# Performance work log

Hardware: AMD Instinct MI355X
Metric: run time of the kernel (lower is better)

Reference implementation:

```python
import jax, jax.numpy as jnp
import numpy as np
import math

B, S, HID, H = 2, 1024, 768, 12
D = HID // H  # 64
ALPHA = 32.0


def setup_inputs() -> dict:
    key = jax.random.key(0)
    ks = jax.random.split(key, 8)
    return {
        "hidden_states": jax.random.normal(ks[0], (B, S, HID), jnp.float32),
        "attention_mask": jnp.zeros((B, 1, 1, S), jnp.float32),
        "head_mask": jnp.ones((1, H, 1, 1), jnp.float32),
        "rel_pos": jax.random.normal(ks[1], (B, H, S, S), jnp.float32),
        "rel_2d_pos": jax.random.normal(ks[2], (B, H, S, S), jnp.float32),
        "Wq": jax.random.normal(ks[3], (HID, HID), jnp.float32) * 0.02,
        "bq": jnp.zeros((HID,), jnp.float32),
        "Wk": jax.random.normal(ks[4], (HID, HID), jnp.float32) * 0.02,
        "bk": jnp.zeros((HID,), jnp.float32),
        "Wv": jax.random.normal(ks[5], (HID, HID), jnp.float32) * 0.02,
        "bv": jnp.zeros((HID,), jnp.float32),
    }


def _heads(x):
    # [B,S,HID] -> [B,H,S,D]
    return x.reshape(B, S, H, D).transpose(0, 2, 1, 3)


def cogview_softmax(scores, alpha=ALPHA):
    s = scores / alpha
    m = jnp.max(s, axis=-1, keepdims=True)
    return jax.nn.softmax((s - m) * alpha, axis=-1)


def reference(hidden_states, attention_mask, head_mask, rel_pos, rel_2d_pos,
              Wq, bq, Wk, bk, Wv, bv):
    norm = math.sqrt(D)
    q = _heads(hidden_states @ Wq + bq) / norm   # [B,H,S,D]
    k = _heads(hidden_states @ Wk + bk)
    v = _heads(hidden_states @ Wv + bv)
    scores = jnp.einsum("bhsd,bhtd->bhst", q, k)
    scores = scores + (rel_pos + rel_2d_pos) / norm
    scores = scores + attention_mask
    probs = cogview_softmax(scores)              # [B,H,S,S]
    probs = probs * head_mask
    ctx = jnp.einsum("bhst,bhtd->bhsd", probs, v)
    ctx = ctx.transpose(0, 2, 1, 3).reshape(B, S, HID)
    return ctx
```

## Files before the change

kernel.cpp:

```cpp
#include <hip/hip_runtime.h>
#include <hip/hip_bf16.h>
#include <cstdint>

#define BB   2
#define SS   1024
#define HIDD 768
#define NH   12
#define DH   64
#define BH   (BB*NH)

typedef short bf16x8 __attribute__((ext_vector_type(8)));
typedef float f32x4  __attribute__((ext_vector_type(4)));

__device__ __forceinline__ unsigned short f2b(float x) {
    union { float f; uint32_t u; } v; v.f = x;
    uint32_t u = v.u;
    uint32_t r = (u + 0x7fffu + ((u >> 16) & 1u)) >> 16;
    return (unsigned short)r;
}

__device__ __forceinline__ void async16(const void* g, void* l) {
    __builtin_amdgcn_global_load_lds(
        (const __attribute__((address_space(1))) unsigned int*)g,
        (__attribute__((address_space(3))) unsigned int*)l,
        16, 0, 0);
}

__global__ void cvt_x(const float* __restrict__ x, unsigned short* __restrict__ xb) {
    int i = blockIdx.x * blockDim.x + threadIdx.x;
    float4 v = ((const float4*)x)[i];
    ushort4 o;
    o.x = f2b(v.x); o.y = f2b(v.y); o.z = f2b(v.z); o.w = f2b(v.w);
    ((ushort4*)xb)[i] = o;
}

__global__ void transpose_w(const float* __restrict__ Wq, const float* __restrict__ Wk,
                            const float* __restrict__ Wv, unsigned short* __restrict__ Wt) {
    __shared__ float tile[32][33];
    const int w = blockIdx.z;
    const float* W = (w == 0) ? Wq : (w == 1) ? Wk : Wv;
    const int tx = threadIdx.x & 31, ty = threadIdx.x >> 5;
    const int k0 = blockIdx.x * 32, n0 = blockIdx.y * 32;
    for (int p = 0; p < 4; ++p)
        tile[ty + p * 8][tx] = W[(k0 + ty + p * 8) * HIDD + n0 + tx];
    __syncthreads();
    for (int p = 0; p < 4; ++p) {
        int n = n0 + ty + p * 8;
        Wt[(w * HIDD + n) * HIDD + k0 + tx] = f2b(tile[tx][ty + p * 8]);
    }
}

__global__ __launch_bounds__(256) void qkv_gemm(
    const unsigned short* __restrict__ Xb, const unsigned short* __restrict__ Wt,
    const float* __restrict__ bq, const float* __restrict__ bk, const float* __restrict__ bv,
    unsigned short* __restrict__ Qh, unsigned short* __restrict__ Kh,
    unsigned short* __restrict__ Vh) {
    __shared__ __align__(16) unsigned short lA[2][128 * 32];
    __shared__ __align__(16) unsigned short lB[2][64 * 32];
    const int t = threadIdx.x;
    const int wave = t >> 6, lane = t & 63;
    const int l15 = lane & 15, quad = lane >> 4;
    const int m0 = blockIdx.x * 128;
    const int n0 = blockIdx.y * 64;
    const int wm = wave * 32;

    f32x4 acc[2][4] = {};

    auto stage = [&](int k0, int b) {
        #pragma unroll
        for (int r = 0; r < 2; ++r) {
            int ci = r * 256 + t;
            async16(Xb + (m0 + (ci >> 2)) * HIDD + k0 + (ci & 3) * 8,
                    &lA[b][(r * 256 + wave * 64) * 8]);
        }
        async16(Wt + (n0 + (t >> 2)) * HIDD + k0 + (t & 3) * 8,
                &lB[b][(wave * 64) * 8]);
    };

    stage(0, 0);
    for (int ki = 0; ki < 24; ++ki) {
        const int cur = ki & 1;
        __syncthreads();
        if (ki < 23) stage((ki + 1) * 32, cur ^ 1);
        bf16x8 af[2], bf[4];
        #pragma unroll
        for (int i = 0; i < 2; ++i)
            af[i] = *(const bf16x8*)&lA[cur][(wm + i * 16 + l15) * 32 + quad * 8];
        #pragma unroll
        for (int j = 0; j < 4; ++j)
            bf[j] = *(const bf16x8*)&lB[cur][(j * 16 + l15) * 32 + quad * 8];
        #pragma unroll
        for (int i = 0; i < 2; ++i)
            #pragma unroll
            for (int j = 0; j < 4; ++j)
                acc[i][j] = __builtin_amdgcn_mfma_f32_16x16x32_bf16(af[i], bf[j], acc[i][j], 0, 0, 0);
    }

    const int sect = (n0 >= 1536) ? 2 : (n0 >= 768) ? 1 : 0;
    const float* bias = (sect == 0) ? bq : (sect == 1) ? bk : bv;
    unsigned short* dst = (sect == 0) ? Qh : (sect == 1) ? Kh : Vh;
    const float scale = (sect == 0) ? 0.125f : 1.0f;
    #pragma unroll
    for (int i = 0; i < 2; ++i) {
        #pragma unroll
        for (int j = 0; j < 4; ++j) {
            int n  = n0 + j * 16 + l15;
            int nn = n - sect * HIDD;
            int h = nn >> 6, d = nn & 63;
            float bval = bias[nn];
            #pragma unroll
            for (int r = 0; r < 4; ++r) {
                int m = m0 + wm + i * 16 + quad * 4 + r;
                int b = m >> 10, s = m & 1023;
                float v = (acc[i][j][r] + bval) * scale;
                dst[((size_t)(b * NH + h) * SS + s) * DH + d] = f2b(v);
            }
        }
    }
}

__global__ __launch_bounds__(256) void transpose_v(
    const unsigned short* __restrict__ Vh, unsigned short* __restrict__ VhT) {
    __shared__ unsigned short tile[64][65];
    const int t = threadIdx.x;
    const int bh = blockIdx.y;
    const int s0 = blockIdx.x * 64;
    const int tx = t & 63, ty = t >> 6;
    const unsigned short* src = Vh + (size_t)bh * SS * DH;
    #pragma unroll
    for (int p = 0; p < 16; ++p)
        tile[ty + p * 4][tx] = src[(size_t)(s0 + ty + p * 4) * DH + tx];
    __syncthreads();
    unsigned short* dst = VhT + (size_t)bh * DH * SS;
    #pragma unroll
    for (int p = 0; p < 16; ++p)
        dst[(size_t)(ty + p * 4) * SS + s0 + tx] = tile[tx][ty + p * 4];
}

__global__ __launch_bounds__(128) void flash_attn(
    const unsigned short* __restrict__ Qh, const unsigned short* __restrict__ Kh,
    const unsigned short* __restrict__ VhT,
    const float* __restrict__ rel, const float* __restrict__ rel2d,
    const float* __restrict__ amask, const float* __restrict__ hmask,
    float* __restrict__ out) {
    __shared__ __align__(16) char smemraw[53760];

    const int t = threadIdx.x;
    const int wave = t >> 6, lane = t & 63;
    const int l15 = lane & 15, quad = lane >> 4;
    const int l7 = l15 & 7;
    const int bh = blockIdx.y;
    const int b = bh / NH, h = bh % NH;
    const int m0w = blockIdx.x * 32 + wave * 16;

    const unsigned short* Qp = Qh + (size_t)bh * SS * DH;
    const unsigned short* Kp = Kh + (size_t)bh * SS * DH;
    const unsigned short* Vp = VhT + (size_t)bh * DH * SS;
    const float* relp  = rel   + (size_t)bh * SS * SS;
    const float* rel2p = rel2d + (size_t)bh * SS * SS;
    const float* maskp = amask + (size_t)b * SS;

    float* stgA = (float*)(smemraw + 32768 + wave * 8192);
    float* stgB = stgA + 1024;
    unsigned short* Pw = (unsigned short*)(smemraw + 49152) + wave * (16 * 72);

    auto stage_kv = [&](int j0, int buf) {
        unsigned short* dK = (unsigned short*)(smemraw + buf * 8192);
        unsigned short* dV = (unsigned short*)(smemraw + 16384 + buf * 8192);
        #pragma unroll
        for (int i = 0; i < 4; ++i) {
            int ci = i * 128 + t;
            int row = ci >> 3, sc = ci & 7;
            int g = sc ^ (row & 7);
            async16(Kp + (size_t)(j0 + row) * DH + g * 8,
                    dK + (i * 128 + wave * 64) * 8);
            async16(Vp + (size_t)row * SS + j0 + g * 8,
                    dV + (i * 128 + wave * 64) * 8);
        }
    };

    auto stage_bias = [&](int j0) {
        #pragma unroll
        for (int i = 0; i < 4; ++i) {
            async16(relp  + (size_t)(m0w + 4 * i + quad) * SS + j0 + l15 * 4,
                    (char*)stgA + i * 1024);
            async16(rel2p + (size_t)(m0w + 4 * i + quad) * SS + j0 + l15 * 4,
                    (char*)stgB + i * 1024);
        }
    };

    bf16x8 qf0 = *(const bf16x8*)&Qp[(m0w + l15) * DH + quad * 8];
    bf16x8 qf1 = *(const bf16x8*)&Qp[(m0w + l15) * DH + 32 + quad * 8];

    f32x4 o[4] = {};
    float mrow[4] = {-1e30f, -1e30f, -1e30f, -1e30f};
    float lrow[4] = {0.f, 0.f, 0.f, 0.f};

    stage_kv(0, 0);
    __syncthreads();

    for (int tt = 0; tt < 16; ++tt) {
        const int j0 = tt * 64, cur = tt & 1;
        const unsigned short* cK = (const unsigned short*)(smemraw + cur * 8192);
        const unsigned short* cV = (const unsigned short*)(smemraw + 16384 + cur * 8192);

        stage_bias(j0);
        if (tt < 15) stage_kv(j0 + 64, cur ^ 1);

        float mk[4];
        #pragma unroll
        for (int c = 0; c < 4; ++c) mk[c] = maskp[j0 + c * 16 + l15];

        f32x4 sc4[4] = {};
        #pragma unroll
        for (int c = 0; c < 4; ++c) {
            int row = c * 16 + l15;
            bf16x8 k0f = *(const bf16x8*)&cK[row * 64 + (quad ^ l7) * 8];
            bf16x8 k1f = *(const bf16x8*)&cK[row * 64 + ((quad + 4) ^ l7) * 8];
            sc4[c] = __builtin_amdgcn_mfma_f32_16x16x32_bf16(qf0, k0f, sc4[c], 0, 0, 0);
            sc4[c] = __builtin_amdgcn_mfma_f32_16x16x32_bf16(qf1, k1f, sc4[c], 0, 0, 0);
        }

        if (tt < 15) { asm volatile("s_waitcnt vmcnt(8)" ::: "memory"); }
        else         { asm volatile("s_waitcnt vmcnt(0)" ::: "memory"); }

        float sv[4][4];
        #pragma unroll
        for (int c = 0; c < 4; ++c)
            #pragma unroll
            for (int r = 0; r < 4; ++r) {
                int fi = (quad * 4 + r) * 64 + c * 16 + l15;
                sv[c][r] = sc4[c][r] + (stgA[fi] + stgB[fi]) * 0.125f + mk[c];
            }

        float alpha[4];
        #pragma unroll
        for (int r = 0; r < 4; ++r) {
            float mx = fmaxf(fmaxf(sv[0][r], sv[1][r]), fmaxf(sv[2][r], sv[3][r]));
            #pragma unroll
            for (int off = 1; off < 16; off <<= 1) mx = fmaxf(mx, __shfl_xor(mx, off, 64));
            float mnew = fmaxf(mrow[r], mx);
            alpha[r] = __expf(mrow[r] - mnew);
            mrow[r] = mnew;
            float rs = 0.f;
            #pragma unroll
            for (int c = 0; c < 4; ++c) {
                float p = __expf(sv[c][r] - mnew);
                sv[c][r] = p;
                rs += p;
            }
            #pragma unroll
            for (int off = 1; off < 16; off <<= 1) rs += __shfl_xor(rs, off, 64);
            lrow[r] = lrow[r] * alpha[r] + rs;
            o[0][r] *= alpha[r]; o[1][r] *= alpha[r]; o[2][r] *= alpha[r]; o[3][r] *= alpha[r];
        }

        #pragma unroll
        for (int c = 0; c < 4; ++c)
            #pragma unroll
            for (int r = 0; r < 4; ++r)
                Pw[(quad * 4 + r) * 72 + c * 16 + l15] = f2b(sv[c][r]);

        bf16x8 pf0 = *(const bf16x8*)&Pw[l15 * 72 + quad * 8];
        bf16x8 pf1 = *(const bf16x8*)&Pw[l15 * 72 + 32 + quad * 8];

        #pragma unroll
        for (int dt = 0; dt < 4; ++dt) {
            int row = dt * 16 + l15;
            bf16x8 v0f = *(const bf16x8*)&cV[row * 64 + (quad ^ l7) * 8];
            bf16x8 v1f = *(const bf16x8*)&cV[row * 64 + ((quad + 4) ^ l7) * 8];
            o[dt] = __builtin_amdgcn_mfma_f32_16x16x32_bf16(pf0, v0f, o[dt], 0, 0, 0);
            o[dt] = __builtin_amdgcn_mfma_f32_16x16x32_bf16(pf1, v1f, o[dt], 0, 0, 0);
        }

        __syncthreads();
    }

    const float hm = hmask[h];
    #pragma unroll
    for (int r = 0; r < 4; ++r) {
        float inv = hm / lrow[r];
        int s = m0w + quad * 4 + r;
        float* op = out + ((size_t)(b * SS + s)) * HIDD + h * DH;
        #pragma unroll
        for (int dt = 0; dt < 4; ++dt) op[dt * 16 + l15] = o[dt][r] * inv;
    }
}

extern "C" void kernel_launch(void* const* d_in, const int* in_sizes, int n_in,
                              void* d_out, int out_size, void* d_ws, size_t ws_size,
                              hipStream_t stream) {
    const float* hs    = (const float*)d_in[0];
    const float* am    = (const float*)d_in[1];
    const float* hm    = (const float*)d_in[2];
    const float* rel   = (const float*)d_in[3];
    const float* rel2d = (const float*)d_in[4];
    const float* Wq    = (const float*)d_in[5];
    const float* bq    = (const float*)d_in[6];
    const float* Wk    = (const float*)d_in[7];
    const float* bk    = (const float*)d_in[8];
    const float* Wv    = (const float*)d_in[9];
    const float* bv    = (const float*)d_in[10];
    float* out = (float*)d_out;

    unsigned short* Xb  = (unsigned short*)d_ws;
    unsigned short* Wt  = Xb + 2048 * HIDD;
    unsigned short* Qh  = Wt + 3 * HIDD * HIDD;
    unsigned short* Kh  = Qh + (size_t)BH * SS * DH;
    unsigned short* Vh  = Kh + (size_t)BH * SS * DH;
    unsigned short* VhT = Vh + (size_t)BH * SS * DH;

    cvt_x<<<(2048 * HIDD / 4) / 256, 256, 0, stream>>>(hs, Xb);
    dim3 gT(24, 24, 3);
    transpose_w<<<gT, 256, 0, stream>>>(Wq, Wk, Wv, Wt);
    dim3 gG(16, 36);
    qkv_gemm<<<gG, 256, 0, stream>>>(Xb, Wt, bq, bk, bv, Qh, Kh, Vh);
    dim3 gV(16, BH);
    transpose_v<<<gV, 256, 0, stream>>>(Vh, VhT);
    dim3 gF(32, BH);
    flash_attn<<<gF, 128, 0, stream>>>(Qh, Kh, VhT, rel, rel2d, am, hm, out);
}
```

Measured before the change: 274.7 us.

## Prefetch relative-position bias directly into registers instead of LDS staging

```diff
diff --git a/kernel.cpp b/kernel.cpp
--- a/kernel.cpp
+++ b/kernel.cpp
@@ -143,7 +143,7 @@
     const float* __restrict__ rel, const float* __restrict__ rel2d,
     const float* __restrict__ amask, const float* __restrict__ hmask,
     float* __restrict__ out) {
-    __shared__ __align__(16) char smemraw[53760];
+    __shared__ __align__(16) char smemraw[37376];
 
     const int t = threadIdx.x;
     const int wave = t >> 6, lane = t & 63;
@@ -160,9 +160,15 @@
     const float* rel2p = rel2d + (size_t)bh * SS * SS;
     const float* maskp = amask + (size_t)b * SS;
 
-    float* stgA = (float*)(smemraw + 32768 + wave * 8192);
-    float* stgB = stgA + 1024;
-    unsigned short* Pw = (unsigned short*)(smemraw + 49152) + wave * (16 * 72);
+    unsigned short* Pw = (unsigned short*)(smemraw + 32768) + wave * (16 * 72);
+
+    const float* rowA[4];
+    const float* rowB[4];
+    #pragma unroll
+    for (int r = 0; r < 4; ++r) {
+        rowA[r] = relp  + (size_t)(m0w + quad * 4 + r) * SS + l15;
+        rowB[r] = rel2p + (size_t)(m0w + quad * 4 + r) * SS + l15;
+    }
 
     auto stage_kv = [&](int j0, int buf) {
         unsigned short* dK = (unsigned short*)(smemraw + buf * 8192);
@@ -179,16 +185,6 @@
         }
     };
 
-    auto stage_bias = [&](int j0) {
-        #pragma unroll
-        for (int i = 0; i < 4; ++i) {
-            async16(relp  + (size_t)(m0w + 4 * i + quad) * SS + j0 + l15 * 4,
-                    (char*)stgA + i * 1024);
-            async16(rel2p + (size_t)(m0w + 4 * i + quad) * SS + j0 + l15 * 4,
-                    (char*)stgB + i * 1024);
-        }
-    };
-
     bf16x8 qf0 = *(const bf16x8*)&Qp[(m0w + l15) * DH + quad * 8];
     bf16x8 qf1 = *(const bf16x8*)&Qp[(m0w + l15) * DH + 32 + quad * 8];
 
@@ -196,16 +192,34 @@
     float mrow[4] = {-1e30f, -1e30f, -1e30f, -1e30f};
     float lrow[4] = {0.f, 0.f, 0.f, 0.f};
 
+    float A0[4][4], B0[4][4], A1[4][4], B1[4][4];
+
+    #pragma unroll
+    for (int r = 0; r < 4; ++r)
+        #pragma unroll
+        for (int c = 0; c < 4; ++c) {
+            A0[r][c] = rowA[r][c * 16];
+            B0[r][c] = rowB[r][c * 16];
+        }
     stage_kv(0, 0);
     __syncthreads();
 
-    for (int tt = 0; tt < 16; ++tt) {
+    auto body = [&](int tt, float (&cA)[4][4], float (&cB)[4][4],
+                    float (&nA)[4][4], float (&nB)[4][4]) {
         const int j0 = tt * 64, cur = tt & 1;
         const unsigned short* cK = (const unsigned short*)(smemraw + cur * 8192);
         const unsigned short* cV = (const unsigned short*)(smemraw + 16384 + cur * 8192);
 
-        stage_bias(j0);
-        if (tt < 15) stage_kv(j0 + 64, cur ^ 1);
+        if (tt < 15) {
+            #pragma unroll
+            for (int r = 0; r < 4; ++r)
+                #pragma unroll
+                for (int c = 0; c < 4; ++c) {
+                    nA[r][c] = rowA[r][j0 + 64 + c * 16];
+                    nB[r][c] = rowB[r][j0 + 64 + c * 16];
+                }
+            stage_kv(j0 + 64, cur ^ 1);
+        }
 
         float mk[4];
         #pragma unroll
@@ -221,17 +235,12 @@
             sc4[c] = __builtin_amdgcn_mfma_f32_16x16x32_bf16(qf1, k1f, sc4[c], 0, 0, 0);
         }
 
-        if (tt < 15) { asm volatile("s_waitcnt vmcnt(8)" ::: "memory"); }
-        else         { asm volatile("s_waitcnt vmcnt(0)" ::: "memory"); }
-
         float sv[4][4];
         #pragma unroll
         for (int c = 0; c < 4; ++c)
             #pragma unroll
-            for (int r = 0; r < 4; ++r) {
-                int fi = (quad * 4 + r) * 64 + c * 16 + l15;
-                sv[c][r] = sc4[c][r] + (stgA[fi] + stgB[fi]) * 0.125f + mk[c];
-            }
+            for (int r = 0; r < 4; ++r)
+                sv[c][r] = sc4[c][r] + (cA[r][c] + cB[r][c]) * 0.125f + mk[c];
 
         float alpha[4];
         #pragma unroll
@@ -274,6 +283,11 @@
         }
 
         __syncthreads();
+    };
+
+    for (int tt = 0; tt < 16; tt += 2) {
+        body(tt,     A0, B0, A1, B1);
+        body(tt + 1, A1, B1, A0, B0);
     }
 
     const float hm = hmask[h];
```

Result: no change. 278.2 us (+1.3%).

## Prefetch rel-pos bias in 128-column chunks with swizzled LDS and custom waitcnt barriers

Applied to the files above, without the earlier changes.

```diff
diff --git a/kernel.cpp b/kernel.cpp
--- a/kernel.cpp
+++ b/kernel.cpp
@@ -143,7 +143,7 @@
     const float* __restrict__ rel, const float* __restrict__ rel2d,
     const float* __restrict__ amask, const float* __restrict__ hmask,
     float* __restrict__ out) {
-    __shared__ __align__(16) char smemraw[53760];
+    __shared__ __align__(16) char smemraw[70144];
 
     const int t = threadIdx.x;
     const int wave = t >> 6, lane = t & 63;
@@ -160,9 +160,10 @@
     const float* rel2p = rel2d + (size_t)bh * SS * SS;
     const float* maskp = amask + (size_t)b * SS;
 
-    float* stgA = (float*)(smemraw + 32768 + wave * 8192);
-    float* stgB = stgA + 1024;
-    unsigned short* Pw = (unsigned short*)(smemraw + 49152) + wave * (16 * 72);
+    char* biasW = smemraw + 32768 + wave * 16384;
+    const float* bA = (const float*)biasW;
+    const float* bB = (const float*)(biasW + 8192);
+    unsigned short* Pw = (unsigned short*)(smemraw + 65536) + wave * (16 * 72);
 
     auto stage_kv = [&](int j0, int buf) {
         unsigned short* dK = (unsigned short*)(smemraw + buf * 8192);
@@ -179,13 +180,15 @@
         }
     };
 
-    auto stage_bias = [&](int j0) {
-        #pragma unroll
-        for (int i = 0; i < 4; ++i) {
-            async16(relp  + (size_t)(m0w + 4 * i + quad) * SS + j0 + l15 * 4,
-                    (char*)stgA + i * 1024);
-            async16(rel2p + (size_t)(m0w + 4 * i + quad) * SS + j0 + l15 * 4,
-                    (char*)stgB + i * 1024);
+    auto stage_bias = [&](int g) {
+        const int j0g = g * 128;
+        #pragma unroll
+        for (int i = 0; i < 8; ++i) {
+            int row = 2 * i + (lane >> 5);
+            int cs  = (lane & 31) ^ ((row >> 2) << 2);
+            size_t off = (size_t)(m0w + row) * SS + j0g + cs * 4;
+            async16(relp  + off, biasW + i * 1024);
+            async16(rel2p + off, biasW + 8192 + i * 1024);
         }
     };
 
@@ -197,14 +200,17 @@
     float lrow[4] = {0.f, 0.f, 0.f, 0.f};
 
     stage_kv(0, 0);
-    __syncthreads();
+    stage_bias(0);
+    asm volatile("s_waitcnt vmcnt(0)" ::: "memory");
+    __builtin_amdgcn_s_barrier();
 
     for (int tt = 0; tt < 16; ++tt) {
-        const int j0 = tt * 64, cur = tt & 1;
+        const int cur = tt & 1;
+        const int T = tt & 1;
+        const int j0 = tt * 64;
         const unsigned short* cK = (const unsigned short*)(smemraw + cur * 8192);
         const unsigned short* cV = (const unsigned short*)(smemraw + 16384 + cur * 8192);
 
-        stage_bias(j0);
         if (tt < 15) stage_kv(j0 + 64, cur ^ 1);
 
         float mk[4];
@@ -212,6 +218,7 @@
         for (int c = 0; c < 4; ++c) mk[c] = maskp[j0 + c * 16 + l15];
 
         f32x4 sc4[4] = {};
+        __builtin_amdgcn_s_setprio(1);
         #pragma unroll
         for (int c = 0; c < 4; ++c) {
             int row = c * 16 + l15;
@@ -220,18 +227,23 @@
             sc4[c] = __builtin_amdgcn_mfma_f32_16x16x32_bf16(qf0, k0f, sc4[c], 0, 0, 0);
             sc4[c] = __builtin_amdgcn_mfma_f32_16x16x32_bf16(qf1, k1f, sc4[c], 0, 0, 0);
         }
-
-        if (tt < 15) { asm volatile("s_waitcnt vmcnt(8)" ::: "memory"); }
-        else         { asm volatile("s_waitcnt vmcnt(0)" ::: "memory"); }
+        __builtin_amdgcn_s_setprio(0);
+
+        if (T == 0) asm volatile("s_waitcnt vmcnt(8)" ::: "memory");
 
         float sv[4][4];
         #pragma unroll
         for (int c = 0; c < 4; ++c)
             #pragma unroll
             for (int r = 0; r < 4; ++r) {
-                int fi = (quad * 4 + r) * 64 + c * 16 + l15;
-                sv[c][r] = sc4[c][r] + (stgA[fi] + stgB[fi]) * 0.125f + mk[c];
+                int row = quad * 4 + r;
+                int idx = row * 128
+                        + ((((T * 16 + c * 4 + (l15 >> 2)) ^ (quad << 2))) << 2)
+                        + (l15 & 3);
+                sv[c][r] = sc4[c][r] + (bA[idx] + bB[idx]) * 0.125f + mk[c];
             }
+
+        if (T == 1 && tt < 15) stage_bias((tt >> 1) + 1);
 
         float alpha[4];
         #pragma unroll
@@ -264,6 +276,7 @@
         bf16x8 pf0 = *(const bf16x8*)&Pw[l15 * 72 + quad * 8];
         bf16x8 pf1 = *(const bf16x8*)&Pw[l15 * 72 + 32 + quad * 8];
 
+        __builtin_amdgcn_s_setprio(1);
         #pragma unroll
         for (int dt = 0; dt < 4; ++dt) {
             int row = dt * 16 + l15;
@@ -272,8 +285,13 @@
             o[dt] = __builtin_amdgcn_mfma_f32_16x16x32_bf16(pf0, v0f, o[dt], 0, 0, 0);
             o[dt] = __builtin_amdgcn_mfma_f32_16x16x32_bf16(pf1, v1f, o[dt], 0, 0, 0);
         }
-
-        __syncthreads();
+        __builtin_amdgcn_s_setprio(0);
+
+        if (tt < 15) {
+            if (T == 0) asm volatile("s_waitcnt vmcnt(0)"  ::: "memory");
+            else        asm volatile("s_waitcnt vmcnt(16)" ::: "memory");
+            __builtin_amdgcn_s_barrier();
+        }
     }
 
     const float hm = hmask[h];
```

Result: slower. 290.6 us (+5.8%).

## Precompute combined fp16 attention bias and stream it async into flash attention

Applied to the files above, without the earlier changes.

```diff
diff --git a/kernel.cpp b/kernel.cpp
--- a/kernel.cpp
+++ b/kernel.cpp
@@ -11,6 +11,7 @@
 
 typedef short bf16x8 __attribute__((ext_vector_type(8)));
 typedef float f32x4  __attribute__((ext_vector_type(4)));
+typedef _Float16 f16x8 __attribute__((ext_vector_type(8)));
 
 __device__ __forceinline__ unsigned short f2b(float x) {
     union { float f; uint32_t u; } v; v.f = x;
@@ -24,6 +25,35 @@
         (const __attribute__((address_space(1))) unsigned int*)g,
         (__attribute__((address_space(3))) unsigned int*)l,
         16, 0, 0);
+}
+
+__global__ __launch_bounds__(256) void prep_bias(
+    const float* __restrict__ rel, const float* __restrict__ rel2d,
+    const float* __restrict__ amask, _Float16* __restrict__ Bh) {
+    const size_t nchunk = (size_t)BH * SS * SS / 8;
+    for (size_t i = blockIdx.x * 256 + threadIdx.x; i < nchunk;
+         i += (size_t)gridDim.x * 256) {
+        const size_t e = i * 8;
+        const int bh = (int)(i >> 17);
+        const int b  = (bh >= NH) ? 1 : 0;
+        const int k8 = ((int)i & 127) * 8;
+        const float4* r1 = (const float4*)(rel + e);
+        const float4* r2 = (const float4*)(rel2d + e);
+        const float4* mp = (const float4*)(amask + (size_t)b * SS + k8);
+        float4 a0 = r1[0], a1 = r1[1];
+        float4 c0 = r2[0], c1 = r2[1];
+        float4 m0 = mp[0], m1 = mp[1];
+        f16x8 o;
+        o[0] = (_Float16)((a0.x + c0.x) * 0.125f + m0.x);
+        o[1] = (_Float16)((a0.y + c0.y) * 0.125f + m0.y);
+        o[2] = (_Float16)((a0.z + c0.z) * 0.125f + m0.z);
+        o[3] = (_Float16)((a0.w + c0.w) * 0.125f + m0.w);
+        o[4] = (_Float16)((a1.x + c1.x) * 0.125f + m1.x);
+        o[5] = (_Float16)((a1.y + c1.y) * 0.125f + m1.y);
+        o[6] = (_Float16)((a1.z + c1.z) * 0.125f + m1.z);
+        o[7] = (_Float16)((a1.w + c1.w) * 0.125f + m1.w);
+        *(f16x8*)(Bh + e) = o;
+    }
 }
 
 __global__ void cvt_x(const float* __restrict__ x, unsigned short* __restrict__ xb) {
@@ -137,7 +167,153 @@
         dst[(size_t)(ty + p * 4) * SS + s0 + tx] = tile[tx][ty + p * 4];
 }
 
-__global__ __launch_bounds__(128) void flash_attn(
+__global__ __launch_bounds__(128) void flash_attn_pb(
+    const unsigned short* __restrict__ Qh, const unsigned short* __restrict__ Kh,
+    const unsigned short* __restrict__ VhT, const _Float16* __restrict__ Bh,
+    const float* __restrict__ hmask, float* __restrict__ out) {
+    __shared__ __align__(16) char smemraw[53760];
+
+    const int t = threadIdx.x;
+    const int wave = t >> 6, lane = t & 63;
+    const int l15 = lane & 15, quad = lane >> 4;
+    const int l7 = l15 & 7;
+    const int bh = blockIdx.y;
+    const int b = bh / NH, h = bh % NH;
+    const int m0w = blockIdx.x * 32 + wave * 16;
+
+    const unsigned short* Qp = Qh + (size_t)bh * SS * DH;
+    const unsigned short* Kp = Kh + (size_t)bh * SS * DH;
+    const unsigned short* Vp = VhT + (size_t)bh * DH * SS;
+    const _Float16* Bhp = Bh + (size_t)bh * SS * SS;
+
+    char* biasW = smemraw + 32768 + wave * 8192;
+    unsigned short* Pw = (unsigned short*)(smemraw + 49152) + wave * (16 * 72);
+
+    auto stage_kv = [&](int j0, int buf) {
+        unsigned short* dK = (unsigned short*)(smemraw + buf * 8192);
+        unsigned short* dV = (unsigned short*)(smemraw + 16384 + buf * 8192);
+        #pragma unroll
+        for (int i = 0; i < 4; ++i) {
+            int ci = i * 128 + t;
+            int row = ci >> 3, sc = ci & 7;
+            int g = sc ^ (row & 7);
+            async16(Kp + (size_t)(j0 + row) * DH + g * 8,
+                    dK + (i * 128 + wave * 64) * 8);
+            async16(Vp + (size_t)row * SS + j0 + g * 8,
+                    dV + (i * 128 + wave * 64) * 8);
+        }
+    };
+
+    auto stage_bias = [&](int g, int gb) {
+        char* dst = biasW + gb * 4096;
+        #pragma unroll
+        for (int i = 0; i < 4; ++i)
+            async16(Bhp + (size_t)(m0w + 4 * i + quad) * SS + g * 128 + l15 * 8,
+                    dst + i * 1024);
+    };
+
+    bf16x8 qf0 = *(const bf16x8*)&Qp[(m0w + l15) * DH + quad * 8];
+    bf16x8 qf1 = *(const bf16x8*)&Qp[(m0w + l15) * DH + 32 + quad * 8];
+
+    f32x4 o[4] = {};
+    float mrow[4] = {-1e30f, -1e30f, -1e30f, -1e30f};
+    float lrow[4] = {0.f, 0.f, 0.f, 0.f};
+
+    stage_kv(0, 0);
+    stage_bias(0, 0);
+    asm volatile("s_waitcnt vmcnt(0)" ::: "memory");
+    __builtin_amdgcn_s_barrier();
+
+    for (int tt = 0; tt < 16; ++tt) {
+        const int cur = tt & 1;
+        const int T = tt & 1;
+        const int g = tt >> 1;
+        const int j0 = tt * 64;
+        const unsigned short* cK = (const unsigned short*)(smemraw + cur * 8192);
+        const unsigned short* cV = (const unsigned short*)(smemraw + 16384 + cur * 8192);
+        const bool pre_bias = (T == 0) && (tt <= 12);
+
+        if (tt < 15) stage_kv(j0 + 64, cur ^ 1);
+        if (pre_bias) stage_bias(g + 1, (g + 1) & 1);
+
+        f32x4 sc4[4] = {};
+        #pragma unroll
+        for (int c = 0; c < 4; ++c) {
+            int row = c * 16 + l15;
+            bf16x8 k0f = *(const bf16x8*)&cK[row * 64 + (quad ^ l7) * 8];
+            bf16x8 k1f = *(const bf16x8*)&cK[row * 64 + ((quad + 4) ^ l7) * 8];
+            sc4[c] = __builtin_amdgcn_mfma_f32_16x16x32_bf16(qf0, k0f, sc4[c], 0, 0, 0);
+            sc4[c] = __builtin_amdgcn_mfma_f32_16x16x32_bf16(qf1, k1f, sc4[c], 0, 0, 0);
+        }
+
+        const _Float16* bl = (const _Float16*)(biasW + (g & 1) * 4096);
+        float sv[4][4];
+        #pragma unroll
+        for (int c = 0; c < 4; ++c)
+            #pragma unroll
+            for (int r = 0; r < 4; ++r)
+                sv[c][r] = sc4[c][r]
+                         + (float)bl[(quad * 4 + r) * 128 + T * 64 + c * 16 + l15];
+
+        float alpha[4];
+        #pragma unroll
+        for (int r = 0; r < 4; ++r) {
+            float mx = fmaxf(fmaxf(sv[0][r], sv[1][r]), fmaxf(sv[2][r], sv[3][r]));
+            #pragma unroll
+            for (int off = 1; off < 16; off <<= 1) mx = fmaxf(mx, __shfl_xor(mx, off, 64));
+            float mnew = fmaxf(mrow[r], mx);
+            alpha[r] = __expf(mrow[r] - mnew);
+            mrow[r] = mnew;
+            float rs = 0.f;
+            #pragma unroll
+            for (int c = 0; c < 4; ++c) {
+                float p = __expf(sv[c][r] - mnew);
+                sv[c][r] = p;
+                rs += p;
+            }
+            #pragma unroll
+            for (int off = 1; off < 16; off <<= 1) rs += __shfl_xor(rs, off, 64);
+            lrow[r] = lrow[r] * alpha[r] + rs;
+            o[0][r] *= alpha[r]; o[1][r] *= alpha[r]; o[2][r] *= alpha[r]; o[3][r] *= alpha[r];
+        }
+
+        #pragma unroll
+        for (int c = 0; c < 4; ++c)
+            #pragma unroll
+            for (int r = 0; r < 4; ++r)
+                Pw[(quad * 4 + r) * 72 + c * 16 + l15] = f2b(sv[c][r]);
+
+        bf16x8 pf0 = *(const bf16x8*)&Pw[l15 * 72 + quad * 8];
+        bf16x8 pf1 = *(const bf16x8*)&Pw[l15 * 72 + 32 + quad * 8];
+
+        #pragma unroll
+        for (int dt = 0; dt < 4; ++dt) {
+            int row = dt * 16 + l15;
+            bf16x8 v0f = *(const bf16x8*)&cV[row * 64 + (quad ^ l7) * 8];
+            bf16x8 v1f = *(const bf16x8*)&cV[row * 64 + ((quad + 4) ^ l7) * 8];
+            o[dt] = __builtin_amdgcn_mfma_f32_16x16x32_bf16(pf0, v0f, o[dt], 0, 0, 0);
+            o[dt] = __builtin_amdgcn_mfma_f32_16x16x32_bf16(pf1, v1f, o[dt], 0, 0, 0);
+        }
+
+        if (tt < 15) {
+            if (pre_bias) asm volatile("s_waitcnt vmcnt(4)" ::: "memory");
+            else          asm volatile("s_waitcnt vmcnt(0)" ::: "memory");
+            __builtin_amdgcn_s_barrier();
+        }
+    }
+
+    const float hm = hmask[h];
+    #pragma unroll
+    for (int r = 0; r < 4; ++r) {
+        float inv = hm / lrow[r];
+        int s = m0w + quad * 4 + r;
+        float* op = out + ((size_t)(b * SS + s)) * HIDD + h * DH;
+        #pragma unroll
+        for (int dt = 0; dt < 4; ++dt) op[dt * 16 + l15] = o[dt][r] * inv;
+    }
+}
+
+__global__ __launch_bounds__(128) void flash_attn_v0(
     const unsigned short* __restrict__ Qh, const unsigned short* __restrict__ Kh,
     const unsigned short* __restrict__ VhT,
     const float* __restrict__ rel, const float* __restrict__ rel2d,
@@ -309,7 +485,13 @@
     unsigned short* Kh  = Qh + (size_t)BH * SS * DH;
     unsigned short* Vh  = Kh + (size_t)BH * SS * DH;
     unsigned short* VhT = Vh + (size_t)BH * SS * DH;
-
+    _Float16* Bh = (_Float16*)(VhT + (size_t)BH * SS * DH);
+
+    const size_t WS_NEEDED = 19267584ULL + 50331648ULL;
+    const bool use_prep = (ws_size >= WS_NEEDED);
+
+    if (use_prep)
+        prep_bias<<<3072, 256, 0, stream>>>(rel, rel2d, am, Bh);
     cvt_x<<<(2048 * HIDD / 4) / 256, 256, 0, stream>>>(hs, Xb);
     dim3 gT(24, 24, 3);
     transpose_w<<<gT, 256, 0, stream>>>(Wq, Wk, Wv, Wt);
@@ -318,5 +500,8 @@
     dim3 gV(16, BH);
     transpose_v<<<gV, 256, 0, stream>>>(Vh, VhT);
     dim3 gF(32, BH);
-    flash_attn<<<gF, 128, 0, stream>>>(Qh, Kh, VhT, rel, rel2d, am, hm, out);
-}
+    if (use_prep)
+        flash_attn_pb<<<gF, 128, 0, stream>>>(Qh, Kh, VhT, Bh, hm, out);
+    else
+        flash_attn_v0<<<gF, 128, 0, stream>>>(Qh, Kh, VhT, rel, rel2d, am, hm, out);
+}
```

Result: slower. 310.5 us (+13.0%).
